# Performance work log

Hardware: AMD Instinct MI355X
Metric: run time of the kernel (lower is better)

## Reference

```python
import jax, jax.numpy as jnp
import numpy as np

B, C, H, W = 8, 512, 64, 64
TEMB = 512
HIDDEN = 1024  # int(C * prompt_hidden_ratio=2.0)
K = C // 2     # max(1, int(C * topk_ratio=0.5))


def silu(x):
    return x * jax.nn.sigmoid(x)


def conv1x1(h, w, b):
    # h: [b,c,hh,ww], w: [out,in], b: [out]
    return jnp.einsum('bchw,oc->bohw', h, w) + b[None, :, None, None]


def setup_inputs() -> dict:
    key = jax.random.key(0)
    ks = jax.random.split(key, 12)
    s = 0.02  # small init so softmax/attention stay well-conditioned
    return {
        'x': jax.random.normal(ks[0], (B, C, H, W), jnp.float32),
        'temb': jax.random.normal(ks[1], (B, TEMB), jnp.float32),
        'w_affine': jax.random.normal(ks[2], (2 * C, TEMB), jnp.float32) * s,
        'b_affine': jnp.zeros((2 * C,), jnp.float32),
        'w_tp': jax.random.normal(ks[3], (C, TEMB), jnp.float32) * s,
        'b_tp': jnp.zeros((C,), jnp.float32),
        'w_m1': jax.random.normal(ks[4], (HIDDEN, 2 * C), jnp.float32) * s,
        'b_m1': jnp.zeros((HIDDEN,), jnp.float32),
        'w_m2': jax.random.normal(ks[5], (C, HIDDEN), jnp.float32) * s,
        'b_m2': jnp.zeros((C,), jnp.float32),
        'wq': jax.random.normal(ks[6], (C, C), jnp.float32) * s,
        'bq': jnp.zeros((C,), jnp.float32),
        'wk': jax.random.normal(ks[7], (C, C), jnp.float32) * s,
        'bk': jnp.zeros((C,), jnp.float32),
        'wv': jax.random.normal(ks[8], (C, C), jnp.float32) * s,
        'bv': jnp.zeros((C,), jnp.float32),
        'wo': jax.random.normal(ks[9], (C, C), jnp.float32) * s,
        'bo': jnp.zeros((C,), jnp.float32),
    }


def reference(x, temb, w_affine, b_affine, w_tp, b_tp, w_m1, b_m1, w_m2, b_m2,
              wq, bq, wk, bk, wv, bv, wo, bo):
    b, c, hgt, wgt = x.shape
    hw = hgt * wgt

    # TimeScaleShift
    temb_act = silu(temb)
    ss = temb_act @ w_affine.T + b_affine              # [b, 2c]
    scale, shift = jnp.split(ss, 2, axis=1)
    h = x * (1.0 + scale[:, :, None, None]) + shift[:, :, None, None]

    # channel prompt
    gap = h.mean(axis=(2, 3))                          # [b, c]
    time_prompt = temb_act @ w_tp.T + b_tp             # [b, c]
    pm = jnp.concatenate([gap, time_prompt], axis=1)   # [b, 2c]
    prompt = silu(pm @ w_m1.T + b_m1) @ w_m2.T + b_m2  # [b, c]

    # top-k channel selection
    _, topk_idx = jax.lax.top_k(prompt, K)             # [b, K] int32

    # q/k/v 1x1 convs, then gather selected channels
    qf = conv1x1(h, wq, bq).reshape(b, c, hw)
    kf = conv1x1(h, wk, bk).reshape(b, c, hw)
    vf = conv1x1(h, wv, bv).reshape(b, c, hw)
    idx3 = topk_idx[:, :, None]
    q = jnp.take_along_axis(qf, idx3, axis=1)          # [b, K, hw]
    k_feat = jnp.take_along_axis(kf, idx3, axis=1)
    v = jnp.take_along_axis(vf, idx3, axis=1)

    # channel attention on the selected subset
    attn = jnp.einsum('bkn,bln->bkl', q, k_feat) * (K ** -0.5)  # [b, K, K]
    attn = jax.nn.softmax(attn, axis=2)
    out = jnp.einsum('bkl,bln->bkn', attn, v)                   # [b, K, hw]

    # scatter back into a zero tensor at the selected channels
    out_full = jax.vmap(
        lambda o, i: jnp.zeros((c, hw), o.dtype).at[i].set(o)
    )(out, topk_idx).reshape(b, c, hgt, wgt)

    return conv1x1(out_full, wo, bo)
```

## Files before the change

kernel.cpp:

```cpp
#include <hip/hip_runtime.h>
#include <hip/hip_bf16.h>
#include <math.h>

typedef __hip_bfloat16 bf16;
typedef __bf16 bf16x8 __attribute__((ext_vector_type(8)));
typedef float f32x4 __attribute__((ext_vector_type(4)));

static __device__ __forceinline__ float b2f(bf16 v) { return __bfloat162float(v); }
static __device__ __forceinline__ bf16 f2b(float v) { return __float2bfloat16(v); }

#define GLOAD16(g, l) __builtin_amdgcn_global_load_lds( \
    (const __attribute__((address_space(1))) void*)(g), \
    (__attribute__((address_space(3))) void*)(l), 16, 0, 0)


#define TM 128
#define TN 64
#define TK 32

template <typename TOUT>
__global__ __launch_bounds__(256) void gemm_bt(
    const bf16* __restrict__ A, size_t sA,
    const bf16* __restrict__ Bt, size_t sB,
    const float* __restrict__ bias, size_t sBias, int hasBias,
    TOUT* __restrict__ D, size_t sD,
    int M, int N, int Kd, int transStore, int NXB)
{
    const int id = blockIdx.x;
    const int bz = id & 7;
    const int slot = id >> 3;
    const int bx = slot % NXB, by = slot / NXB;

    A  += (size_t)bz * sA;
    Bt += (size_t)bz * sB;
    D  += (size_t)bz * sD;
    if (hasBias) bias += (size_t)bz * sBias;

    const int m0 = by * TM, n0 = bx * TN;
    const int t = threadIdx.x, wv = t >> 6, lane = t & 63;
    const int lr = lane & 15, quad = lane >> 4;
    const int qx8 = (quad ^ ((lr >> 1) & 3)) * 8;

    __shared__ bf16 lA[2][TM * TK];
    __shared__ bf16 lB[2][TN * TK];

    f32x4 acc[2][4];
#pragma unroll
    for (int i = 0; i < 2; ++i)
#pragma unroll
        for (int j = 0; j < 4; ++j) acc[i][j] = (f32x4){0.f, 0.f, 0.f, 0.f};

    const int srow = lane >> 2;
    const int scol = ((lane & 3) ^ ((lane >> 3) & 3)) * 8;
    const bf16* as0 = A  + (size_t)(m0 + wv * 16 + srow) * Kd + scol;
    const bf16* bs0 = Bt + (size_t)(n0 + wv * 16 + srow) * Kd + scol;

    GLOAD16(as0, &lA[0][wv * 512]);
    GLOAD16(as0 + (size_t)64 * Kd, &lA[0][wv * 512 + 2048]);
    GLOAD16(bs0, &lB[0][wv * 512]);
    __syncthreads();

    int cur = 0;
    for (int k0 = 0; k0 < Kd; k0 += TK) {
        const int kn = k0 + TK;
        if (kn < Kd) {
            GLOAD16(as0 + kn, &lA[cur ^ 1][wv * 512]);
            GLOAD16(as0 + (size_t)64 * Kd + kn, &lA[cur ^ 1][wv * 512 + 2048]);
            GLOAD16(bs0 + kn, &lB[cur ^ 1][wv * 512]);
        }
        const bf16* bA = lA[cur];
        const bf16* bB = lB[cur];
        bf16x8 af0 = *(const bf16x8*)(bA + (wv * 32 + lr) * 32 + qx8);
        bf16x8 af1 = *(const bf16x8*)(bA + (wv * 32 + 16 + lr) * 32 + qx8);
#pragma unroll
        for (int j = 0; j < 4; ++j) {
            bf16x8 bfj = *(const bf16x8*)(bB + (j * 16 + lr) * 32 + qx8);
            acc[0][j] = __builtin_amdgcn_mfma_f32_16x16x32_bf16(af0, bfj, acc[0][j], 0, 0, 0);
            acc[1][j] = __builtin_amdgcn_mfma_f32_16x16x32_bf16(af1, bfj, acc[1][j], 0, 0, 0);
        }
        __syncthreads();
        cur ^= 1;
    }

#pragma unroll
    for (int i = 0; i < 2; ++i) {
        const int mb = m0 + wv * 32 + i * 16 + quad * 4;
#pragma unroll
        for (int r = 0; r < 4; ++r) {
            const int mm = mb + r;
            const float bvv = hasBias ? bias[mm] : 0.f;
#pragma unroll
            for (int j = 0; j < 4; ++j) {
                const int nn = n0 + j * 16 + lr;
                const float v = acc[i][j][r] + bvv;
                const size_t o = transStore ? ((size_t)nn * M + mm)
                                            : ((size_t)mm * N + nn);
                if constexpr (__is_same(TOUT, float)) D[o] = v;
                else                                  D[o] = f2b(v);
            }
        }
    }
}

__global__ __launch_bounds__(256) void k_prep(const float* __restrict__ x,
                                              bf16* __restrict__ xT,
                                              float* __restrict__ xsump)
{
    const int b = blockIdx.z;
    const int c0 = blockIdx.y * 64;
    const int n0 = blockIdx.x * 512;
    const int t = threadIdx.x;
    const int cr = t >> 2;
    const int sub = t & 3;
    __shared__ bf16 tile[64][72];

    const float* xrow = x + ((size_t)b * 512 + c0 + cr) * 4096 + n0 + sub * 16;
    float s = 0.f;

    for (int st = 0; st < 8; ++st) {
        __syncthreads();
        float4 f[4];
#pragma unroll
        for (int q = 0; q < 4; ++q) f[q] = *(const float4*)(xrow + st * 64 + q * 4);
#pragma unroll
        for (int q = 0; q < 4; ++q) {
            s += f[q].x + f[q].y + f[q].z + f[q].w;
            union { bf16 h[4]; uint2 u; } p;
            p.h[0] = f2b(f[q].x); p.h[1] = f2b(f[q].y);
            p.h[2] = f2b(f[q].z); p.h[3] = f2b(f[q].w);
            *(uint2*)&tile[cr][sub * 16 + q * 4] = p.u;
        }
        __syncthreads();
        union { bf16 h[8]; uint4 u; } o0, o1;
#pragma unroll
        for (int i = 0; i < 8; ++i) o0.h[i] = tile[sub * 16 + i][cr];
#pragma unroll
        for (int i = 0; i < 8; ++i) o1.h[i] = tile[sub * 16 + 8 + i][cr];
        bf16* orow = xT + ((size_t)b * 4096 + n0 + st * 64 + cr) * 512 + c0 + sub * 16;
        *(uint4*)(orow)     = o0.u;
        *(uint4*)(orow + 8) = o1.u;
    }
    s += __shfl_down(s, 2);
    s += __shfl_down(s, 1);
    if (sub == 0) xsump[(size_t)blockIdx.x * 4096 + b * 512 + c0 + cr] = s;
}

__global__ __launch_bounds__(256) void gemm_qkv2(
    const bf16* __restrict__ Aall, const bf16* __restrict__ xT,
    const float* __restrict__ bias,
    bf16* __restrict__ qb, bf16* __restrict__ kb, bf16* __restrict__ vT)
{
    const int id = blockIdx.x;
    const int b = id & 7;
    const int slot = id >> 3;
    const int mt = slot % 6;
    const int n0 = (slot / 6) * 128;

    const bf16* A  = Aall + (size_t)b * 393216 + (size_t)mt * 65536;
    const bf16* Bt = xT + (size_t)b * 2097152;
    bias += b * 768 + mt * 128;

    const int t = threadIdx.x, w = t >> 6, lane = t & 63;
    const int lr = lane & 15, quad = lane >> 4;
    const int wr = w >> 1, wc = w & 1;
    const int qx8 = (quad ^ ((lr >> 1) & 3)) * 8;

    __shared__ bf16 lA[2][128 * 32];
    __shared__ bf16 lB[2][128 * 32];

    f32x4 acc[4][4];
#pragma unroll
    for (int i = 0; i < 4; ++i)
#pragma unroll
        for (int j = 0; j < 4; ++j) acc[i][j] = (f32x4){0.f, 0.f, 0.f, 0.f};

    const int srow = lane >> 2;
    const int scol = ((lane & 3) ^ ((lane >> 3) & 3)) * 8;
    const bf16* as0 = A  + (size_t)(w * 16 + srow) * 512 + scol;
    const bf16* bs0 = Bt + (size_t)(n0 + w * 16 + srow) * 512 + scol;

    GLOAD16(as0, &lA[0][w * 512]);
    GLOAD16(as0 + 32768, &lA[0][w * 512 + 2048]);
    GLOAD16(bs0, &lB[0][w * 512]);
    GLOAD16(bs0 + 32768, &lB[0][w * 512 + 2048]);
    __syncthreads();

    int cur = 0;
    for (int k0 = 0; k0 < 512; k0 += 32) {
        const int kn = k0 + 32;
        if (kn < 512) {
            GLOAD16(as0 + kn, &lA[cur ^ 1][w * 512]);
            GLOAD16(as0 + 32768 + kn, &lA[cur ^ 1][w * 512 + 2048]);
            GLOAD16(bs0 + kn, &lB[cur ^ 1][w * 512]);
            GLOAD16(bs0 + 32768 + kn, &lB[cur ^ 1][w * 512 + 2048]);
        }
        const bf16* bA = lA[cur];
        const bf16* bB = lB[cur];
        bf16x8 af[4], bfr[4];
#pragma unroll
        for (int i = 0; i < 4; ++i)
            af[i] = *(const bf16x8*)(bA + (wr * 64 + i * 16 + lr) * 32 + qx8);
#pragma unroll
        for (int j = 0; j < 4; ++j)
            bfr[j] = *(const bf16x8*)(bB + (wc * 64 + j * 16 + lr) * 32 + qx8);
#pragma unroll
        for (int i = 0; i < 4; ++i)
#pragma unroll
            for (int j = 0; j < 4; ++j)
                acc[i][j] = __builtin_amdgcn_mfma_f32_16x16x32_bf16(af[i], bfr[j], acc[i][j], 0, 0, 0);
        __syncthreads();
        cur ^= 1;
    }

#pragma unroll
    for (int i = 0; i < 4; ++i) {
        const int mq = wr * 64 + i * 16 + quad * 4;
#pragma unroll
        for (int r = 0; r < 4; ++r) {
            const int ml = mq + r;
            const float bvv = bias[ml];
            const int mmg = mt * 128 + ml;
            const int mloc = mmg & 255;
#pragma unroll
            for (int j = 0; j < 4; ++j) {
                const int nn = n0 + wc * 64 + j * 16 + lr;
                const float v = acc[i][j][r] + bvv;
                if (mmg < 256)      qb[(size_t)b * 1048576 + (size_t)mloc * 4096 + nn] = f2b(v);
                else if (mmg < 512) kb[(size_t)b * 1048576 + (size_t)mloc * 4096 + nn] = f2b(v);
                else                vT[(size_t)b * 1048576 + (size_t)nn * 256 + mloc] = f2b(v);
            }
        }
    }
}

__global__ __launch_bounds__(256) void gemm_s_splitk(
    const bf16* __restrict__ qb, const bf16* __restrict__ kb,
    float* __restrict__ part)
{
    const int id = blockIdx.x;
    const int b = id & 7;
    const int slot = id >> 3;
    const int s = slot >> 3;
    const int rem = slot & 7;
    const int m0 = (rem >> 2) * TM, n0 = (rem & 3) * TN;

    const bf16* A  = qb + (size_t)b * 1048576;
    const bf16* Bt = kb + (size_t)b * 1048576;

    const int t = threadIdx.x, wv = t >> 6, lane = t & 63;
    const int lr = lane & 15, quad = lane >> 4;
    const int qx8 = (quad ^ ((lr >> 1) & 3)) * 8;

    __shared__ bf16 lA[2][TM * TK];
    __shared__ bf16 lB[2][TN * TK];

    f32x4 acc[2][4];
#pragma unroll
    for (int i = 0; i < 2; ++i)
#pragma unroll
        for (int j = 0; j < 4; ++j) acc[i][j] = (f32x4){0.f, 0.f, 0.f, 0.f};

    const int srow = lane >> 2;
    const int scol = ((lane & 3) ^ ((lane >> 3) & 3)) * 8;
    const bf16* as0 = A  + (size_t)(m0 + wv * 16 + srow) * 4096 + scol;
    const bf16* bs0 = Bt + (size_t)(n0 + wv * 16 + srow) * 4096 + scol;

    const int kBeg = s * 512, kEnd = kBeg + 512;

    GLOAD16(as0 + kBeg, &lA[0][wv * 512]);
    GLOAD16(as0 + (size_t)64 * 4096 + kBeg, &lA[0][wv * 512 + 2048]);
    GLOAD16(bs0 + kBeg, &lB[0][wv * 512]);
    __syncthreads();

    int cur = 0;
    for (int k0 = kBeg; k0 < kEnd; k0 += TK) {
        const int kn = k0 + TK;
        if (kn < kEnd) {
            GLOAD16(as0 + kn, &lA[cur ^ 1][wv * 512]);
            GLOAD16(as0 + (size_t)64 * 4096 + kn, &lA[cur ^ 1][wv * 512 + 2048]);
            GLOAD16(bs0 + kn, &lB[cur ^ 1][wv * 512]);
        }
        const bf16* bA = lA[cur];
        const bf16* bB = lB[cur];
        bf16x8 af0 = *(const bf16x8*)(bA + (wv * 32 + lr) * 32 + qx8);
        bf16x8 af1 = *(const bf16x8*)(bA + (wv * 32 + 16 + lr) * 32 + qx8);
#pragma unroll
        for (int j = 0; j < 4; ++j) {
            bf16x8 bfj = *(const bf16x8*)(bB + (j * 16 + lr) * 32 + qx8);
            acc[0][j] = __builtin_amdgcn_mfma_f32_16x16x32_bf16(af0, bfj, acc[0][j], 0, 0, 0);
            acc[1][j] = __builtin_amdgcn_mfma_f32_16x16x32_bf16(af1, bfj, acc[1][j], 0, 0, 0);
        }
        __syncthreads();
        cur ^= 1;
    }

    float* dst = part + ((size_t)(s * 8 + b) * 256) * 256;
#pragma unroll
    for (int i = 0; i < 2; ++i) {
        const int mb = m0 + wv * 32 + i * 16 + quad * 4;
#pragma unroll
        for (int r = 0; r < 4; ++r) {
            const int mm = mb + r;
#pragma unroll
            for (int j = 0; j < 4; ++j)
                dst[(size_t)mm * 256 + n0 + j * 16 + lr] = acc[i][j][r];
        }
    }
}


__global__ void k_silu(const float* __restrict__ in, float* __restrict__ out, int n)
{
    int i = blockIdx.x * 256 + threadIdx.x;
    if (i < n) {
        float v = in[i];
        out[i] = v / (1.f + expf(-v));
    }
}

__global__ void k_smallgemm(const float* __restrict__ in, const float* __restrict__ W,
                            const float* __restrict__ bias, float* __restrict__ out,
                            int Mrows, int O, int Kd, int act)
{
    const int gw = (blockIdx.x * 256 + threadIdx.x) >> 6;
    const int lane = threadIdx.x & 63;
    if (gw >= Mrows * O) return;
    const int m = gw / O, o = gw - m * O;
    float s = 0.f;
    for (int k = lane; k < Kd; k += 64)
        s += in[m * Kd + k] * W[(size_t)o * Kd + k];
    for (int off = 32; off; off >>= 1) s += __shfl_down(s, off);
    if (lane == 0) {
        s += bias[o];
        if (act) s = s / (1.f + expf(-s));
        out[m * O + o] = s;
    }
}

__global__ void k_mlp1(const float* __restrict__ ss, const float* __restrict__ xsump,
                       const float* __restrict__ tp, const float* __restrict__ w_m1,
                       const float* __restrict__ b_m1, float* __restrict__ hidden)
{
    const int gw = (blockIdx.x * 256 + threadIdx.x) >> 6;
    const int lane = threadIdx.x & 63;
    if (gw >= 8 * 1024) return;
    const int m = gw >> 10, o = gw & 1023;
    float s = 0.f;
    for (int k = lane; k < 1024; k += 64) {
        float pv;
        if (k < 512) {
            float xs = 0.f;
#pragma unroll
            for (int p = 0; p < 8; ++p) xs += xsump[p * 4096 + m * 512 + k];
            pv = (1.f + ss[m * 1024 + k]) * (xs * (1.f / 4096.f))
                 + ss[m * 1024 + 512 + k];
        } else {
            pv = tp[m * 512 + k - 512];
        }
        s += pv * w_m1[(size_t)o * 1024 + k];
    }
    for (int off = 32; off; off >>= 1) s += __shfl_down(s, off);
    if (lane == 0) {
        s += b_m1[o];
        hidden[m * 1024 + o] = s / (1.f + expf(-s));
    }
}

__global__ void k_topk(const float* __restrict__ prompt, int* __restrict__ idx)
{
    __shared__ float v[512];
    __shared__ int sel[512];
    const int b = blockIdx.x, c = threadIdx.x;
    v[c] = prompt[b * 512 + c];
    __syncthreads();
    const float mv = v[c];
    int rank = 0;
    for (int j = 0; j < 512; ++j) {
        float o = v[j];
        rank += (o > mv) || (o == mv && j < c);
    }
    sel[c] = (rank < 256) ? 1 : 0;
    __syncthreads();
    if (rank < 256) {
        int pos = 0;
        for (int j = 0; j < c; ++j) pos += sel[j];
        idx[b * 256 + pos] = c;
    }
}

__global__ void k_gather(const int* __restrict__ idx, const float* __restrict__ ss,
                         const float* __restrict__ wq, const float* __restrict__ wk,
                         const float* __restrict__ wv, const float* __restrict__ wo,
                         bf16* __restrict__ wqkv_g, bf16* __restrict__ wo_g)
{
    const int b = blockIdx.z;
    const int* id = idx + b * 256;
    const int tid = blockIdx.x * 256 + threadIdx.x;
    {
        const int mat = tid >> 17, r = tid & 131071;
        const int j = r >> 9, c = r & 511;
        const int ch = id[j];
        const float* W = mat == 0 ? wq : (mat == 1 ? wk : wv);
        wqkv_g[(size_t)b * 393216 + tid] = f2b(W[ch * 512 + c] * (1.f + ss[b * 1024 + c]));
    }
    if (tid < 131072) {
        const int o = tid >> 8, j = tid & 255;
        wo_g[(size_t)b * 131072 + tid] = f2b(wo[o * 512 + id[j]]);
    }
}

__global__ void k_biasadj(const int* __restrict__ idx, const float* __restrict__ ss,
                          const float* __restrict__ wq, const float* __restrict__ bq,
                          const float* __restrict__ wk, const float* __restrict__ bk,
                          const float* __restrict__ wv, const float* __restrict__ bv,
                          float* __restrict__ bqkv)
{
    const int gw = (blockIdx.x * 256 + threadIdx.x) >> 6;
    const int lane = threadIdx.x & 63;
    if (gw >= 8 * 768) return;
    const int b = gw / 768, j3 = gw - b * 768;
    const int mat = j3 >> 8, j = j3 & 255;
    const int ch = idx[b * 256 + j];
    const float* W  = mat == 0 ? wq : (mat == 1 ? wk : wv);
    const float* Bb = mat == 0 ? bq : (mat == 1 ? bk : bv);
    const float* shift = ss + b * 1024 + 512;
    float s = 0.f;
    for (int c = lane; c < 512; c += 64)
        s += W[(size_t)ch * 512 + c] * shift[c];
    for (int off = 32; off; off >>= 1) s += __shfl_down(s, off);
    if (lane == 0) bqkv[b * 768 + j3] = Bb[ch] + s;
}

__global__ void k_softmax_red(const float* __restrict__ part, bf16* __restrict__ Pt)
{
    const int row = blockIdx.x;
    const int b = row >> 8, j = row & 255;
    const int t = threadIdx.x;
    const int lane = t & 63, wv = t >> 6;
    __shared__ float redm[4], reds[4];
    float v = 0.f;
#pragma unroll
    for (int s = 0; s < 8; ++s)
        v += part[((size_t)(s * 8 + b) * 256 + j) * 256 + t];
    v *= 0.0625f;
    float m = v;
    for (int off = 32; off; off >>= 1) m = fmaxf(m, __shfl_down(m, off));
    if (lane == 0) redm[wv] = m;
    __syncthreads();
    m = fmaxf(fmaxf(redm[0], redm[1]), fmaxf(redm[2], redm[3]));
    const float e = __expf(v - m);
    float s = e;
    for (int off = 32; off; off >>= 1) s += __shfl_down(s, off);
    if (lane == 0) reds[wv] = s;
    __syncthreads();
    s = reds[0] + reds[1] + reds[2] + reds[3];
    Pt[(size_t)b * 65536 + (size_t)t * 256 + j] = f2b(e / s);
}


extern "C" void kernel_launch(void* const* d_in, const int* in_sizes, int n_in,
                              void* d_out, int out_size, void* d_ws, size_t ws_size,
                              hipStream_t stream)
{
    const float* x        = (const float*)d_in[0];
    const float* temb     = (const float*)d_in[1];
    const float* w_affine = (const float*)d_in[2];
    const float* b_affine = (const float*)d_in[3];
    const float* w_tp     = (const float*)d_in[4];
    const float* b_tp     = (const float*)d_in[5];
    const float* w_m1     = (const float*)d_in[6];
    const float* b_m1     = (const float*)d_in[7];
    const float* w_m2     = (const float*)d_in[8];
    const float* b_m2     = (const float*)d_in[9];
    const float* wq       = (const float*)d_in[10];
    const float* bq       = (const float*)d_in[11];
    const float* wk       = (const float*)d_in[12];
    const float* bk       = (const float*)d_in[13];
    const float* wv       = (const float*)d_in[14];
    const float* bv       = (const float*)d_in[15];
    const float* wo       = (const float*)d_in[16];
    const float* bo       = (const float*)d_in[17];
    float* out = (float*)d_out;

    char* ws = (char*)d_ws;
    size_t off = 0;
    auto alloc = [&](size_t bytes) -> char* {
        char* p = ws + off;
        off += (bytes + 255) & ~(size_t)255;
        return p;
    };

    float* temb_act = (float*)alloc(4096 * 4);
    float* ssb      = (float*)alloc(8192 * 4);
    float* tp       = (float*)alloc(4096 * 4);
    float* xsump    = (float*)alloc((size_t)8 * 4096 * 4);
    float* hidden   = (float*)alloc(8192 * 4);
    float* prompt   = (float*)alloc(4096 * 4);
    int*   idx      = (int*)alloc(2048 * 4);
    bf16*  xT     = (bf16*)alloc((size_t)8 * 4096 * 512 * 2);
    float* part   = (float*)alloc((size_t)8 * 8 * 256 * 256 * 4);
    bf16*  wqkv_g = (bf16*)alloc((size_t)8 * 768 * 512 * 2);
    float* bqkv_g = (float*)alloc(8 * 768 * 4);
    bf16*  wo_g   = (bf16*)alloc((size_t)8 * 512 * 256 * 2);
    bf16*  qb     = (bf16*)alloc((size_t)8 * 256 * 4096 * 2);
    bf16*  kb     = (bf16*)alloc((size_t)8 * 256 * 4096 * 2);
    bf16*  vT     = (bf16*)alloc((size_t)8 * 4096 * 256 * 2);
    bf16*  Pt     = (bf16*)alloc((size_t)8 * 256 * 256 * 2);
    bf16*  W2     = (bf16*)alloc((size_t)8 * 512 * 256 * 2);
    (void)ws_size; (void)n_in; (void)in_sizes; (void)out_size;

    k_prep<<<dim3(8, 8, 8), 256, 0, stream>>>(x, xT, xsump);
    k_silu<<<16, 256, 0, stream>>>(temb, temb_act, 4096);
    k_smallgemm<<<2048, 256, 0, stream>>>(temb_act, w_affine, b_affine, ssb, 8, 1024, 512, 0);
    k_smallgemm<<<1024, 256, 0, stream>>>(temb_act, w_tp, b_tp, tp, 8, 512, 512, 0);
    k_mlp1<<<2048, 256, 0, stream>>>(ssb, xsump, tp, w_m1, b_m1, hidden);
    k_smallgemm<<<1024, 256, 0, stream>>>(hidden, w_m2, b_m2, prompt, 8, 512, 1024, 0);
    k_topk<<<8, 512, 0, stream>>>(prompt, idx);
    k_gather<<<dim3(1536, 1, 8), 256, 0, stream>>>(idx, ssb, wq, wk, wv, wo, wqkv_g, wo_g);
    k_biasadj<<<1536, 256, 0, stream>>>(idx, ssb, wq, bq, wk, bk, wv, bv, bqkv_g);
    gemm_qkv2<<<1536, 256, 0, stream>>>(wqkv_g, xT, bqkv_g, qb, kb, vT);
    gemm_s_splitk<<<512, 256, 0, stream>>>(qb, kb, part);
    k_softmax_red<<<2048, 256, 0, stream>>>(part, Pt);
    gemm_bt<bf16><<<128, 256, 0, stream>>>(wo_g, 131072, Pt, 65536,
                                           nullptr, 0, 0,
                                           W2, 131072, 512, 256, 256, 0, 4);
    gemm_bt<float><<<2048, 256, 0, stream>>>(W2, 131072, vT, 1048576,
                                             bo, 0, 1,
                                             out, 2097152, 512, 4096, 256, 0, 64);
}
```

Baseline: 341.4 us.

## Triple-buffer GEMM LDS loads with vmcnt waits and fold SiLU into small GEMM

The three MFMA GEMM kernels move from double to triple LDS buffering. Each iteration prefetches two K-steps ahead and waits with s_waitcnt vmcnt(N) plus a raw s_barrier instead of a full __syncthreads, so global-to-LDS loads overlap more compute. Past the end of K, prefetch addresses wrap and issue harmless loads into unused buffers. Separately, the temb SiLU kernel is removed and its activation is applied inside k_smallgemm, dropping one launch but recomputing the sigmoid per output row.

```diff
diff --git a/kernel.cpp b/kernel.cpp
--- a/kernel.cpp
+++ b/kernel.cpp
@@ -12,6 +12,8 @@
 #define GLOAD16(g, l) __builtin_amdgcn_global_load_lds( \
     (const __attribute__((address_space(1))) void*)(g), \
     (__attribute__((address_space(3))) void*)(l), 16, 0, 0)
+
+#define WAITVM(N) asm volatile("s_waitcnt vmcnt(" #N ")" ::: "memory")
 
 
 #define TM 128
@@ -41,8 +43,8 @@
     const int lr = lane & 15, quad = lane >> 4;
     const int qx8 = (quad ^ ((lr >> 1) & 3)) * 8;
 
-    __shared__ bf16 lA[2][TM * TK];
-    __shared__ bf16 lB[2][TN * TK];
+    __shared__ bf16 lA[3][TM * TK];
+    __shared__ bf16 lB[3][TN * TK];
 
     f32x4 acc[2][4];
 #pragma unroll
@@ -55,19 +57,28 @@
     const bf16* as0 = A  + (size_t)(m0 + wv * 16 + srow) * Kd + scol;
     const bf16* bs0 = Bt + (size_t)(n0 + wv * 16 + srow) * Kd + scol;
 
-    GLOAD16(as0, &lA[0][wv * 512]);
-    GLOAD16(as0 + (size_t)64 * Kd, &lA[0][wv * 512 + 2048]);
-    GLOAD16(bs0, &lB[0][wv * 512]);
-    __syncthreads();
+    const int kd2 = (2 * TK < Kd) ? 2 * TK : 0;
+    {
+        GLOAD16(as0, &lA[0][wv * 512]);
+        GLOAD16(as0 + (size_t)64 * Kd, &lA[0][wv * 512 + 2048]);
+        GLOAD16(bs0, &lB[0][wv * 512]);
+        const int k1 = (TK < Kd) ? TK : 0;
+        GLOAD16(as0 + k1, &lA[1][wv * 512]);
+        GLOAD16(as0 + (size_t)64 * Kd + k1, &lA[1][wv * 512 + 2048]);
+        GLOAD16(bs0 + k1, &lB[1][wv * 512]);
+    }
+    WAITVM(3);
+    __builtin_amdgcn_s_barrier();
 
     int cur = 0;
     for (int k0 = 0; k0 < Kd; k0 += TK) {
-        const int kn = k0 + TK;
-        if (kn < Kd) {
-            GLOAD16(as0 + kn, &lA[cur ^ 1][wv * 512]);
-            GLOAD16(as0 + (size_t)64 * Kd + kn, &lA[cur ^ 1][wv * 512 + 2048]);
-            GLOAD16(bs0 + kn, &lB[cur ^ 1][wv * 512]);
-        }
+        int kn = k0 + 2 * TK; if (kn >= Kd) kn -= Kd;
+        int nx2 = cur + 2; if (nx2 >= 3) nx2 -= 3;
+        GLOAD16(as0 + kn, &lA[nx2][wv * 512]);
+        GLOAD16(as0 + (size_t)64 * Kd + kn, &lA[nx2][wv * 512 + 2048]);
+        GLOAD16(bs0 + kn, &lB[nx2][wv * 512]);
+        (void)kd2;
+
         const bf16* bA = lA[cur];
         const bf16* bB = lB[cur];
         bf16x8 af0 = *(const bf16x8*)(bA + (wv * 32 + lr) * 32 + qx8);
@@ -78,8 +89,9 @@
             acc[0][j] = __builtin_amdgcn_mfma_f32_16x16x32_bf16(af0, bfj, acc[0][j], 0, 0, 0);
             acc[1][j] = __builtin_amdgcn_mfma_f32_16x16x32_bf16(af1, bfj, acc[1][j], 0, 0, 0);
         }
-        __syncthreads();
-        cur ^= 1;
+        WAITVM(3);
+        __builtin_amdgcn_s_barrier();
+        cur = (cur + 1 == 3) ? 0 : cur + 1;
     }
 
 #pragma unroll
@@ -165,8 +177,8 @@
     const int wr = w >> 1, wc = w & 1;
     const int qx8 = (quad ^ ((lr >> 1) & 3)) * 8;
 
-    __shared__ bf16 lA[2][128 * 32];
-    __shared__ bf16 lB[2][128 * 32];
+    __shared__ bf16 lA[3][128 * 32];
+    __shared__ bf16 lB[3][128 * 32];
 
     f32x4 acc[4][4];
 #pragma unroll
@@ -183,17 +195,22 @@
     GLOAD16(as0 + 32768, &lA[0][w * 512 + 2048]);
     GLOAD16(bs0, &lB[0][w * 512]);
     GLOAD16(bs0 + 32768, &lB[0][w * 512 + 2048]);
-    __syncthreads();
+    GLOAD16(as0 + 32, &lA[1][w * 512]);
+    GLOAD16(as0 + 32768 + 32, &lA[1][w * 512 + 2048]);
+    GLOAD16(bs0 + 32, &lB[1][w * 512]);
+    GLOAD16(bs0 + 32768 + 32, &lB[1][w * 512 + 2048]);
+    WAITVM(4);
+    __builtin_amdgcn_s_barrier();
 
     int cur = 0;
     for (int k0 = 0; k0 < 512; k0 += 32) {
-        const int kn = k0 + 32;
-        if (kn < 512) {
-            GLOAD16(as0 + kn, &lA[cur ^ 1][w * 512]);
-            GLOAD16(as0 + 32768 + kn, &lA[cur ^ 1][w * 512 + 2048]);
-            GLOAD16(bs0 + kn, &lB[cur ^ 1][w * 512]);
-            GLOAD16(bs0 + 32768 + kn, &lB[cur ^ 1][w * 512 + 2048]);
-        }
+        int kn = k0 + 64; if (kn >= 512) kn -= 512;
+        int nx2 = cur + 2; if (nx2 >= 3) nx2 -= 3;
+        GLOAD16(as0 + kn, &lA[nx2][w * 512]);
+        GLOAD16(as0 + 32768 + kn, &lA[nx2][w * 512 + 2048]);
+        GLOAD16(bs0 + kn, &lB[nx2][w * 512]);
+        GLOAD16(bs0 + 32768 + kn, &lB[nx2][w * 512 + 2048]);
+
         const bf16* bA = lA[cur];
         const bf16* bB = lB[cur];
         bf16x8 af[4], bfr[4];
@@ -208,8 +225,10 @@
 #pragma unroll
             for (int j = 0; j < 4; ++j)
                 acc[i][j] = __builtin_amdgcn_mfma_f32_16x16x32_bf16(af[i], bfr[j], acc[i][j], 0, 0, 0);
-        __syncthreads();
-        cur ^= 1;
+
+        WAITVM(4);
+        __builtin_amdgcn_s_barrier();
+        cur = (cur + 1 == 3) ? 0 : cur + 1;
     }
 
 #pragma unroll
@@ -251,8 +270,8 @@
     const int lr = lane & 15, quad = lane >> 4;
     const int qx8 = (quad ^ ((lr >> 1) & 3)) * 8;
 
-    __shared__ bf16 lA[2][TM * TK];
-    __shared__ bf16 lB[2][TN * TK];
+    __shared__ bf16 lA[3][TM * TK];
+    __shared__ bf16 lB[3][TN * TK];
 
     f32x4 acc[2][4];
 #pragma unroll
@@ -270,16 +289,20 @@
     GLOAD16(as0 + kBeg, &lA[0][wv * 512]);
     GLOAD16(as0 + (size_t)64 * 4096 + kBeg, &lA[0][wv * 512 + 2048]);
     GLOAD16(bs0 + kBeg, &lB[0][wv * 512]);
-    __syncthreads();
+    GLOAD16(as0 + kBeg + TK, &lA[1][wv * 512]);
+    GLOAD16(as0 + (size_t)64 * 4096 + kBeg + TK, &lA[1][wv * 512 + 2048]);
+    GLOAD16(bs0 + kBeg + TK, &lB[1][wv * 512]);
+    WAITVM(3);
+    __builtin_amdgcn_s_barrier();
 
     int cur = 0;
     for (int k0 = kBeg; k0 < kEnd; k0 += TK) {
-        const int kn = k0 + TK;
-        if (kn < kEnd) {
-            GLOAD16(as0 + kn, &lA[cur ^ 1][wv * 512]);
-            GLOAD16(as0 + (size_t)64 * 4096 + kn, &lA[cur ^ 1][wv * 512 + 2048]);
-            GLOAD16(bs0 + kn, &lB[cur ^ 1][wv * 512]);
-        }
+        int kn = k0 + 2 * TK; if (kn >= kEnd) kn -= 512;
+        int nx2 = cur + 2; if (nx2 >= 3) nx2 -= 3;
+        GLOAD16(as0 + kn, &lA[nx2][wv * 512]);
+        GLOAD16(as0 + (size_t)64 * 4096 + kn, &lA[nx2][wv * 512 + 2048]);
+        GLOAD16(bs0 + kn, &lB[nx2][wv * 512]);
+
         const bf16* bA = lA[cur];
         const bf16* bB = lB[cur];
         bf16x8 af0 = *(const bf16x8*)(bA + (wv * 32 + lr) * 32 + qx8);
@@ -290,8 +313,9 @@
             acc[0][j] = __builtin_amdgcn_mfma_f32_16x16x32_bf16(af0, bfj, acc[0][j], 0, 0, 0);
             acc[1][j] = __builtin_amdgcn_mfma_f32_16x16x32_bf16(af1, bfj, acc[1][j], 0, 0, 0);
         }
-        __syncthreads();
-        cur ^= 1;
+        WAITVM(3);
+        __builtin_amdgcn_s_barrier();
+        cur = (cur + 1 == 3) ? 0 : cur + 1;
     }
 
     float* dst = part + ((size_t)(s * 8 + b) * 256) * 256;
@@ -309,26 +333,20 @@
 }
 
 
-__global__ void k_silu(const float* __restrict__ in, float* __restrict__ out, int n)
-{
-    int i = blockIdx.x * 256 + threadIdx.x;
-    if (i < n) {
-        float v = in[i];
-        out[i] = v / (1.f + expf(-v));
-    }
-}
-
 __global__ void k_smallgemm(const float* __restrict__ in, const float* __restrict__ W,
                             const float* __restrict__ bias, float* __restrict__ out,
-                            int Mrows, int O, int Kd, int act)
+                            int Mrows, int O, int Kd, int act, int inAct)
 {
     const int gw = (blockIdx.x * 256 + threadIdx.x) >> 6;
     const int lane = threadIdx.x & 63;
     if (gw >= Mrows * O) return;
     const int m = gw / O, o = gw - m * O;
     float s = 0.f;
-    for (int k = lane; k < Kd; k += 64)
-        s += in[m * Kd + k] * W[(size_t)o * Kd + k];
+    for (int k = lane; k < Kd; k += 64) {
+        float iv = in[m * Kd + k];
+        if (inAct) iv = iv / (1.f + expf(-iv));
+        s += iv * W[(size_t)o * Kd + k];
+    }
     for (int off = 32; off; off >>= 1) s += __shfl_down(s, off);
     if (lane == 0) {
         s += bias[o];
@@ -490,7 +508,6 @@
         return p;
     };
 
-    float* temb_act = (float*)alloc(4096 * 4);
     float* ssb      = (float*)alloc(8192 * 4);
     float* tp       = (float*)alloc(4096 * 4);
     float* xsump    = (float*)alloc((size_t)8 * 4096 * 4);
@@ -510,11 +527,10 @@
     (void)ws_size; (void)n_in; (void)in_sizes; (void)out_size;
 
     k_prep<<<dim3(8, 8, 8), 256, 0, stream>>>(x, xT, xsump);
-    k_silu<<<16, 256, 0, stream>>>(temb, temb_act, 4096);
-    k_smallgemm<<<2048, 256, 0, stream>>>(temb_act, w_affine, b_affine, ssb, 8, 1024, 512, 0);
-    k_smallgemm<<<1024, 256, 0, stream>>>(temb_act, w_tp, b_tp, tp, 8, 512, 512, 0);
+    k_smallgemm<<<2048, 256, 0, stream>>>(temb, w_affine, b_affine, ssb, 8, 1024, 512, 0, 1);
+    k_smallgemm<<<1024, 256, 0, stream>>>(temb, w_tp, b_tp, tp, 8, 512, 512, 0, 1);
     k_mlp1<<<2048, 256, 0, stream>>>(ssb, xsump, tp, w_m1, b_m1, hidden);
-    k_smallgemm<<<1024, 256, 0, stream>>>(hidden, w_m2, b_m2, prompt, 8, 512, 1024, 0);
+    k_smallgemm<<<1024, 256, 0, stream>>>(hidden, w_m2, b_m2, prompt, 8, 512, 1024, 0, 0);
     k_topk<<<8, 512, 0, stream>>>(prompt, idx);
     k_gather<<<dim3(1536, 1, 8), 256, 0, stream>>>(idx, ssb, wq, wk, wv, wo, wqkv_g, wo_g);
     k_biasadj<<<1536, 256, 0, stream>>>(idx, ssb, wq, bq, wk, bk, wv, bv, bqkv_g);
```

Result: no change. 343.3 us (+0.6%).
